# Optimization experiments

Hardware: AMD Instinct MI355X
Metric: run time of the kernel (lower is better)

The kernel has to match this reference:

```python
import jax, jax.numpy as jnp
import numpy as np

DIM = 384
HEADS = 6
NEG = -1e9  # masked-score fill; equivalent to gathering only kept K/V rows


def setup_inputs() -> dict:
    key = jax.random.key(0)
    ks = jax.random.split(key, 9)
    B, N, C = 1, 4098, DIM
    x = jax.random.normal(ks[0], (B, N, C), dtype=jnp.float32)
    pos = jax.random.normal(ks[1], (B, N + 1, C), dtype=jnp.float32)
    # float mask in [0,1); >=0.5 means 'foreground / keep as key', <0.5 pooled into back token
    mask = jax.random.uniform(ks[2], (B, 1, N - 2), dtype=jnp.float32)
    mask_block = jnp.ones((N + 1,), dtype=jnp.float32)  # positions 0, N-1, N always kept
    Wq = jax.random.normal(ks[3], (C, C), dtype=jnp.float32) * 0.02
    Wk = jax.random.normal(ks[4], (C, C), dtype=jnp.float32) * 0.02
    Wv = jax.random.normal(ks[5], (C, C), dtype=jnp.float32) * 0.02
    Wp = jax.random.normal(ks[6], (C, C), dtype=jnp.float32) * 0.02
    bp = jnp.zeros((C,), dtype=jnp.float32)
    return {"x": x, "pos": pos, "mask": mask, "mask_block": mask_block,
            "Wq": Wq, "Wk": Wk, "Wv": Wv, "Wp": Wp, "bp": bp}


def reference(x, pos, mask, mask_block, Wq, Wk, Wv, Wp, bp):
    B, N, C = x.shape
    H = HEADS
    D = C // H
    scale = D ** -0.5
    eps = 1e-10

    # back token: average of background (mask < 0.5) interior tokens
    reverse = jnp.where(mask < 0.5, 1.0, 0.0)                      # (B,1,N-2)
    pooled = jnp.einsum('bon,bnc->boc', reverse, x[:, 1:N - 1])    # (B,1,C)
    back_tokens = pooled / (reverse.sum(axis=2, keepdims=True) + eps)

    kv_x = jnp.concatenate([x, back_tokens], axis=1)               # (B,N+1,C)
    q_x = x + pos[:, :N]
    k_x = kv_x + pos

    q = (q_x @ Wq.T).reshape(B, N, H, D).transpose(0, 2, 1, 3)       # (B,H,N,D)
    k = (k_x @ Wk.T).reshape(B, N + 1, H, D).transpose(0, 2, 1, 3)   # (B,H,N+1,D)
    v = (kv_x @ Wv.T).reshape(B, N + 1, H, D).transpose(0, 2, 1, 3)  # (B,H,N+1,D)

    # key-selection mask: original gathers rows with mask_block >= 0.5;
    # masked softmax over all N+1 keys is mathematically identical.
    mb = mask_block.at[1:N - 1].set(mask[0, 0])
    keep = mb >= 0.5                                               # (N+1,)

    scores = jnp.einsum('bhqd,bhkd->bhqk', q, k) * scale
    scores = jnp.where(keep[None, None, None, :], scores, NEG)
    attn = jax.nn.softmax(scores, axis=-1)
    out = jnp.einsum('bhqk,bhkd->bhqd', attn, v)
    out = out.transpose(0, 2, 1, 3).reshape(B, N, C)
    return out @ Wp.T + bp
```

## Files before the change

kernel.cpp:

```cpp
#include <hip/hip_runtime.h>
#include <math.h>

#define N_TOK 4098
#define NK_TOK 4099
#define C_DIM 384
#define NKPAD 4160

typedef short  bh8 __attribute__((ext_vector_type(8)));
typedef float  f32x4 __attribute__((ext_vector_type(4)));
typedef unsigned short ushort;
typedef ushort u4 __attribute__((ext_vector_type(4)));
typedef ushort u8 __attribute__((ext_vector_type(8)));

static __device__ __forceinline__ ushort f2bf(float f) {
  unsigned int u = __float_as_uint(f);
  u = (u + 0x7FFF + ((u >> 16) & 1)) >> 16;
  return (ushort)u;
}
static __device__ __forceinline__ float bf2f(ushort s) {
  return __uint_as_float(((unsigned int)s) << 16);
}

typedef const __attribute__((address_space(1))) unsigned int* gas_t;
typedef __attribute__((address_space(3))) unsigned int* las_t;
static __device__ __forceinline__ void gload16(const void* g, void* l) {
  __builtin_amdgcn_global_load_lds((gas_t)g, (las_t)l, 16, 0, 0);
}

static __device__ __forceinline__ void stage_tile(const ushort* src, int rs,
                                                  ushort* lds, int t) {
#pragma unroll
  for (int it = 0; it < 2; ++it) {
    const int base = it * 256 + (t & 192);
    const int i = base + (t & 63);
    const int r = i >> 3, c8 = i & 7;
    gload16(src + r * rs + ((c8 ^ (r & 7)) << 3), lds + base * 8);
  }
}
static __device__ __forceinline__ bh8 frag(const ushort* lds, int row, int c8) {
  return *(const bh8*)&lds[(row << 6) + ((c8 ^ (row & 7)) << 3)];
}

__global__ __launch_bounds__(384) void poolkeep_kernel(
    const float* __restrict__ x, const float* __restrict__ mask,
    const float* __restrict__ mask_block, float* __restrict__ pooled,
    float* __restrict__ cnt, int* __restrict__ nk, int* __restrict__ inv) {
  const int b = blockIdx.x, t = threadIdx.x;
  if (b < 128) {
    const int r0 = b * 32;
    float acc = 0.f;
    int lc = 0;
    for (int r = r0; r < r0 + 32; ++r)
      if (mask[r] < 0.5f) { acc += x[(size_t)(r + 1) * C_DIM + t]; ++lc; }
    atomicAdd(&pooled[t], acc);
    if (t == 0) atomicAdd(cnt, (float)lc);
  } else {
    const int w = t >> 6, lane = t & 63;
    const int span = (b - 128) * 6 + w;
    if (span >= 65) return;
    const int j = span * 64 + lane;
    bool keep = false;
    if (j < NK_TOK)
      keep = (j >= 1 && j <= N_TOK - 2) ? (mask[j - 1] >= 0.5f)
                                        : (mask_block[j] >= 0.5f);
    const unsigned long long bal = __ballot(keep);
    const int pre = __popcll(bal & ((1ull << lane) - 1ull));
    const int c64 = __popcll(bal);
    int base = 0;
    if (lane == 0) base = atomicAdd(nk, c64);
    base = __shfl(base, 0);
    if (j < NK_TOK) inv[j] = keep ? (base + pre) : -1;
  }
}

__global__ __launch_bounds__(256) void prep_kernel(
    const float* __restrict__ x, const float* __restrict__ pos,
    const float* __restrict__ pooled, const float* __restrict__ cnt,
    const float* __restrict__ Wq, const float* __restrict__ Wk,
    const float* __restrict__ Wv, const float* __restrict__ Wp,
    ushort* __restrict__ Aq, ushort* __restrict__ Ak,
    ushort* __restrict__ Av, ushort* __restrict__ Wb) {
  const int b = blockIdx.x, t = threadIdx.x;
  if (b < 65) {
    const int r0 = b * 64;
#pragma unroll 4
    for (int i = 0; i < 24; ++i) {
      const int idx = i * 1024 + t * 4;
      const int row = r0 + idx / C_DIM, col = idx % C_DIM;
      if (row > NK_TOK - 1) continue;
      const float4 pv = *(const float4*)&pos[(size_t)row * C_DIM + col];
      float4 xv;
      if (row == NK_TOK - 1) {
        const float ic = 1.f / (*cnt + 1e-10f);
        xv.x = pooled[col] * ic;     xv.y = pooled[col + 1] * ic;
        xv.z = pooled[col + 2] * ic; xv.w = pooled[col + 3] * ic;
      } else {
        xv = *(const float4*)&x[(size_t)row * C_DIM + col];
      }
      if (row < N_TOK) {
        u4 q4 = {f2bf((xv.x + pv.x) * 0.125f), f2bf((xv.y + pv.y) * 0.125f),
                 f2bf((xv.z + pv.z) * 0.125f), f2bf((xv.w + pv.w) * 0.125f)};
        *(u4*)&Aq[(size_t)row * C_DIM + col] = q4;
      }
      u4 k4 = {f2bf(xv.x + pv.x), f2bf(xv.y + pv.y),
               f2bf(xv.z + pv.z), f2bf(xv.w + pv.w)};
      *(u4*)&Ak[(size_t)row * C_DIM + col] = k4;
      u4 v4 = {f2bf(xv.x), f2bf(xv.y), f2bf(xv.z), f2bf(xv.w)};
      *(u4*)&Av[(size_t)row * C_DIM + col] = v4;
    }
  } else {
    const int wi = b - 65;
    const float* src = (wi < 4) ? Wq : (wi < 8) ? Wk : (wi < 12) ? Wv : Wp;
    const int base = (wi & 3) * 36864;
#pragma unroll 4
    for (int i = 0; i < 36; ++i) {
      const int idx = base + i * 1024 + t * 4;
      const float4 v = *(const float4*)&src[idx];
      u4 o = {f2bf(v.x), f2bf(v.y), f2bf(v.z), f2bf(v.w)};
      *(u4*)&Wb[(size_t)(wi >> 2) * 147456 + idx] = o;
    }
  }
}

static __device__ __forceinline__ void gemm_core(const ushort* A, const ushort* B,
    ushort* As, ushort* Bs, int t, int w, int quad, int l15, f32x4 acc[4]) {
  stage_tile(A, C_DIM, As, t);
  stage_tile(B, C_DIM, Bs, t);
  __syncthreads();
#pragma unroll
  for (int kt = 0; kt < 6; ++kt) {
    const int cur = (kt & 1) << 12;
    if (kt < 5) {
      stage_tile(A + (kt + 1) * 64, C_DIM, As + (cur ^ 4096), t);
      stage_tile(B + (kt + 1) * 64, C_DIM, Bs + (cur ^ 4096), t);
    }
    const bh8 b0 = frag(Bs + cur, w * 16 + l15, quad);
    const bh8 b1 = frag(Bs + cur, w * 16 + l15, 4 + quad);
#pragma unroll
    for (int mb = 0; mb < 4; ++mb) {
      const bh8 a0 = frag(As + cur, mb * 16 + l15, quad);
      const bh8 a1 = frag(As + cur, mb * 16 + l15, 4 + quad);
      acc[mb] = __builtin_amdgcn_mfma_f32_16x16x32_bf16(a0, b0, acc[mb], 0, 0, 0);
      acc[mb] = __builtin_amdgcn_mfma_f32_16x16x32_bf16(a1, b1, acc[mb], 0, 0, 0);
    }
    __syncthreads();
  }
}

__global__ __launch_bounds__(256) void gemm3_kernel(
    const ushort* __restrict__ Aq, const ushort* __restrict__ Ak,
    const ushort* __restrict__ Av, const ushort* __restrict__ Wb,
    const int* __restrict__ inv, ushort* __restrict__ Qh,
    ushort* __restrict__ Kc, ushort* __restrict__ Vc) {
  __shared__ ushort As[8192], Bs[8192];
  const int t = threadIdx.x, w = t >> 6, lane = t & 63;
  const int quad = lane >> 4, l15 = lane & 15;
  const int m0 = blockIdx.x * 64;
  const int which = blockIdx.y / 6, h = blockIdx.y % 6;
  const ushort* A = (which == 0 ? Aq : which == 1 ? Ak : Av) + (size_t)m0 * C_DIM;
  const ushort* B = Wb + (size_t)which * 147456 + (size_t)h * 64 * C_DIM;
  f32x4 acc[4];
#pragma unroll
  for (int i = 0; i < 4; ++i) acc[i] = (f32x4){0.f, 0.f, 0.f, 0.f};
  gemm_core(A, B, As, Bs, t, w, quad, l15, acc);
  const int n = w * 16 + l15;
  if (which == 0) {
#pragma unroll
    for (int mb = 0; mb < 4; ++mb)
#pragma unroll
      for (int r = 0; r < 4; ++r) {
        const int m = m0 + mb * 16 + quad * 4 + r;
        if (m < N_TOK) Qh[((size_t)h * N_TOK + m) * 64 + n] = f2bf(acc[mb][r]);
      }
  } else {
    ushort* dst = (which == 1) ? Kc : Vc;
#pragma unroll
    for (int mb = 0; mb < 4; ++mb)
#pragma unroll
      for (int r = 0; r < 4; ++r) {
        const int m = m0 + mb * 16 + quad * 4 + r;
        if (m < NK_TOK) {
          const int slot = inv[m];
          if (slot >= 0) dst[((size_t)h * NKPAD + slot) * 64 + n] = f2bf(acc[mb][r]);
        }
      }
  }
}

__global__ __launch_bounds__(256) void gemm_out_kernel(
    const ushort* __restrict__ Am, const ushort* __restrict__ Wpb,
    const float* __restrict__ bp, float* __restrict__ out) {
  __shared__ ushort As[8192], Bs[8192];
  const int t = threadIdx.x, w = t >> 6, lane = t & 63;
  const int quad = lane >> 4, l15 = lane & 15;
  const int m0 = blockIdx.x * 64;
  const int h = blockIdx.y;
  f32x4 acc[4];
#pragma unroll
  for (int i = 0; i < 4; ++i) acc[i] = (f32x4){0.f, 0.f, 0.f, 0.f};
  gemm_core(Am + (size_t)m0 * C_DIM, Wpb + (size_t)h * 64 * C_DIM,
            As, Bs, t, w, quad, l15, acc);
  const int n = w * 16 + l15;
  const float bb = bp[h * 64 + n];
#pragma unroll
  for (int mb = 0; mb < 4; ++mb)
#pragma unroll
    for (int r = 0; r < 4; ++r) {
      const int m = m0 + mb * 16 + quad * 4 + r;
      if (m < N_TOK) out[(size_t)m * C_DIM + h * 64 + n] = acc[mb][r] + bb;
    }
}

__global__ __launch_bounds__(256) void vtrans_kernel(const ushort* __restrict__ Vc,
                                                     ushort* __restrict__ Vt) {
  __shared__ ushort T[64][72];
  const int c = blockIdx.x, h = blockIdx.y, t = threadIdx.x;
#pragma unroll
  for (int i = 0; i < 2; ++i) {
    const int s = t + i * 256, r = s >> 3, g = s & 7;
    *(u8*)&T[r][g * 8] =
        *(const u8*)&Vc[((size_t)h * NKPAD + c * 64 + r) * 64 + g * 8];
  }
  __syncthreads();
#pragma unroll
  for (int i = 0; i < 2; ++i) {
    const int s = t + i * 256, d = s >> 3, g = s & 7;
    u8 o;
#pragma unroll
    for (int j = 0; j < 8; ++j) o[j] = T[g * 8 + j][d];
    *(u8*)&Vt[((size_t)h * 64 + d) * NKPAD + c * 64 + g * 8] = o;
  }
}

__global__ __launch_bounds__(256) void attn_kernel(
    const ushort* __restrict__ Qh, const ushort* __restrict__ Kc,
    const ushort* __restrict__ Vt, const int* __restrict__ nkp,
    ushort* __restrict__ Opart, float* __restrict__ Lpart) {
  __shared__ ushort KsB[8192], VsB[8192];
  __shared__ ushort Ps[4][32][72];
  const int t = threadIdx.x, w = t >> 6, lane = t & 63;
  const int quad = lane >> 4, l15 = lane & 15;
  const int h = blockIdx.y, slice = blockIdx.z;
  const int q0 = blockIdx.x * 128;
  const int nk = *nkp, nchunk = (nk + 63) >> 6;

  bh8 qf[2][2];
#pragma unroll
  for (int g = 0; g < 2; ++g) {
    int qr = q0 + w * 32 + g * 16 + l15;
    if (qr > N_TOK - 1) qr = N_TOK - 1;
    const ushort* qp = Qh + ((size_t)h * N_TOK + qr) * 64 + quad * 8;
    qf[g][0] = *(const bh8*)qp;
    qf[g][1] = *(const bh8*)(qp + 32);
  }
  f32x4 oacc[2][4];
#pragma unroll
  for (int g = 0; g < 2; ++g)
#pragma unroll
    for (int i = 0; i < 4; ++i) oacc[g][i] = (f32x4){0.f, 0.f, 0.f, 0.f};
  float l_r[2] = {0.f, 0.f};

  const ushort* kb = Kc + (size_t)h * NKPAD * 64;
  const ushort* vb = Vt + (size_t)h * 64 * NKPAD;

  if (slice < nchunk) {
    stage_tile(kb + (size_t)slice * 4096, 64, KsB, t);
    stage_tile(vb + slice * 64, NKPAD, VsB, t);
  }
  __syncthreads();
  int bsel = 0;
  for (int kc = slice; kc < nchunk; kc += 3) {
    if (kc + 3 < nchunk) {
      stage_tile(kb + (size_t)(kc + 3) * 4096, 64, KsB + ((bsel ^ 1) << 12), t);
      stage_tile(vb + (kc + 3) * 64, NKPAD, VsB + ((bsel ^ 1) << 12), t);
    }
    const ushort* ks = KsB + (bsel << 12);
    const ushort* vs = VsB + (bsel << 12);
#pragma unroll
    for (int g = 0; g < 2; ++g) {
      float csum = 0.f;
#pragma unroll
      for (int f = 0; f < 4; ++f) {
        f32x4 s4 = {0.f, 0.f, 0.f, 0.f};
        const bh8 a0 = frag(ks, f * 16 + l15, quad);
        const bh8 a1 = frag(ks, f * 16 + l15, 4 + quad);
        s4 = __builtin_amdgcn_mfma_f32_16x16x32_bf16(a0, qf[g][0], s4, 0, 0, 0);
        s4 = __builtin_amdgcn_mfma_f32_16x16x32_bf16(a1, qf[g][1], s4, 0, 0, 0);
        const int keyb = kc * 64 + f * 16 + quad * 4;
        u4 pv;
#pragma unroll
        for (int r = 0; r < 4; ++r) {
          const float p = (keyb + r < nk) ? __expf(s4[r]) : 0.f;
          csum += p;
          pv[r] = f2bf(p);
        }
        *(u4*)&Ps[w][g * 16 + l15][f * 16 + quad * 4] = pv;
      }
      csum += __shfl_xor(csum, 16);
      csum += __shfl_xor(csum, 32);
      l_r[g] += csum;
    }
    bh8 pa[2][2];
#pragma unroll
    for (int g = 0; g < 2; ++g) {
      pa[g][0] = *(const bh8*)&Ps[w][g * 16 + l15][quad * 8];
      pa[g][1] = *(const bh8*)&Ps[w][g * 16 + l15][32 + quad * 8];
    }
#pragma unroll
    for (int db = 0; db < 4; ++db) {
      const bh8 b0 = frag(vs, db * 16 + l15, quad);
      const bh8 b1 = frag(vs, db * 16 + l15, 4 + quad);
#pragma unroll
      for (int g = 0; g < 2; ++g) {
        oacc[g][db] = __builtin_amdgcn_mfma_f32_16x16x32_bf16(pa[g][0], b0, oacc[g][db], 0, 0, 0);
        oacc[g][db] = __builtin_amdgcn_mfma_f32_16x16x32_bf16(pa[g][1], b1, oacc[g][db], 0, 0, 0);
      }
    }
    __syncthreads();
    bsel ^= 1;
  }
  const int sh = slice * 6 + h;
#pragma unroll
  for (int g = 0; g < 2; ++g) {
#pragma unroll
    for (int db = 0; db < 4; ++db)
#pragma unroll
      for (int r = 0; r < 4; ++r) {
        const int q = q0 + w * 32 + g * 16 + quad * 4 + r;
        if (q < N_TOK)
          Opart[((size_t)sh * NKPAD + q) * 64 + db * 16 + l15] = f2bf(oacc[g][db][r]);
      }
    if (quad == 0) {
      const int q = q0 + w * 32 + g * 16 + l15;
      if (q < N_TOK) Lpart[sh * NKPAD + q] = l_r[g];
    }
  }
}

__global__ __launch_bounds__(256) void merge_kernel(const ushort* __restrict__ Opart,
                                                    const float* __restrict__ Lpart,
                                                    ushort* __restrict__ Am) {
  const int idx = blockIdx.x * 256 + threadIdx.x;
  if (idx >= N_TOK * 48) return;
  const int q = idx / 48, c = (idx % 48) * 8;
  const int h = c >> 6, d = c & 63;
  float l = 0.f;
#pragma unroll
  for (int s = 0; s < 3; ++s) l += Lpart[(s * 6 + h) * NKPAD + q];
  const float inv = 1.f / l;
  float o[8] = {0.f, 0.f, 0.f, 0.f, 0.f, 0.f, 0.f, 0.f};
#pragma unroll
  for (int s = 0; s < 3; ++s) {
    const u8 v = *(const u8*)&Opart[((size_t)(s * 6 + h) * NKPAD + q) * 64 + d];
#pragma unroll
    for (int j = 0; j < 8; ++j) o[j] += bf2f(v[j]);
  }
  u8 r;
#pragma unroll
  for (int j = 0; j < 8; ++j) r[j] = f2bf(o[j] * inv);
  *(u8*)&Am[(size_t)q * C_DIM + c] = r;
}

extern "C" void kernel_launch(void* const* d_in, const int* in_sizes, int n_in,
                              void* d_out, int out_size, void* d_ws, size_t ws_size,
                              hipStream_t stream) {
  const float* x          = (const float*)d_in[0];
  const float* pos        = (const float*)d_in[1];
  const float* mask       = (const float*)d_in[2];
  const float* mask_block = (const float*)d_in[3];
  const float* Wq         = (const float*)d_in[4];
  const float* Wk         = (const float*)d_in[5];
  const float* Wv         = (const float*)d_in[6];
  const float* Wp         = (const float*)d_in[7];
  const float* bp         = (const float*)d_in[8];
  float* out = (float*)d_out;
  char* wsb = (char*)d_ws;

  float*  pooled = (float*)wsb;
  float*  cnt    = (float*)(wsb + 1536);
  int*    nk     = (int*)(wsb + 1540);
  int*    inv    = (int*)(wsb + 2048);
  ushort* Aq     = (ushort*)(wsb + 20480);
  ushort* Ak     = (ushort*)(wsb + 3215360);
  ushort* Av     = (ushort*)(wsb + 6410240);
  ushort* Wb     = (ushort*)(wsb + 9605120);
  ushort* Qh     = (ushort*)(wsb + 10784768);
  ushort* Kc     = (ushort*)(wsb + 13932032);
  ushort* Vc     = (ushort*)(wsb + 17126912);
  ushort* Vt     = (ushort*)(wsb + 20321792);
  float*  Lp     = (float*)(wsb + 23516672);
  ushort* Am     = (ushort*)(wsb + 23816192);
  ushort* Op     = Aq;

  hipMemsetAsync(d_ws, 0, 2048, stream);
  poolkeep_kernel<<<dim3(139), dim3(384), 0, stream>>>(x, mask, mask_block,
                                                       pooled, cnt, nk, inv);
  prep_kernel<<<dim3(81), dim3(256), 0, stream>>>(x, pos, pooled, cnt,
                                                  Wq, Wk, Wv, Wp, Aq, Ak, Av, Wb);
  gemm3_kernel<<<dim3(65, 18), 256, 0, stream>>>(Aq, Ak, Av, Wb, inv, Qh, Kc, Vc);
  vtrans_kernel<<<dim3(65, 6), 256, 0, stream>>>(Vc, Vt);
  attn_kernel<<<dim3(33, 6, 3), 256, 0, stream>>>(Qh, Kc, Vt, nk, Op, Lp);
  merge_kernel<<<dim3(769), 256, 0, stream>>>(Op, Lp, Am);
  gemm_out_kernel<<<dim3(65, 6), 256, 0, stream>>>(Am, Wb + 3 * 147456, bp, out);
}
```

Before: 166.2 us.

## Cut kernel launches: fuse V transpose, merge into attention, drop memset and atomics

Removes the memset, the V-transpose kernel and the merge kernel. gemm3 now writes V directly in transposed layout, and the last attention slice block for each (q-tile, head) does the 3-way partial merge, chosen through an atomic counter with threadfences. Pooling now writes per-block partials that prep reduces. The keep-index scan moves into prep as a block-level prefix sum, and prep uses more, smaller blocks. This saves launch overhead and intermediate round trips, at the cost of strided scattered stores for Vt and a serial pooled reduction in one prep block, which the other 255 row blocks do not wait on (block 256 alone handles the back-token row).

```diff
diff --git a/kernel.cpp b/kernel.cpp
--- a/kernel.cpp
+++ b/kernel.cpp
@@ -41,62 +41,57 @@
   return *(const bh8*)&lds[(row << 6) + ((c8 ^ (row & 7)) << 3)];
 }
 
-__global__ __launch_bounds__(384) void poolkeep_kernel(
+__global__ __launch_bounds__(384) void pool_kernel(
     const float* __restrict__ x, const float* __restrict__ mask,
-    const float* __restrict__ mask_block, float* __restrict__ pooled,
-    float* __restrict__ cnt, int* __restrict__ nk, int* __restrict__ inv) {
+    float* __restrict__ pooled_part, float* __restrict__ cnt_part,
+    int* __restrict__ done) {
   const int b = blockIdx.x, t = threadIdx.x;
-  if (b < 128) {
-    const int r0 = b * 32;
-    float acc = 0.f;
-    int lc = 0;
-    for (int r = r0; r < r0 + 32; ++r)
-      if (mask[r] < 0.5f) { acc += x[(size_t)(r + 1) * C_DIM + t]; ++lc; }
-    atomicAdd(&pooled[t], acc);
-    if (t == 0) atomicAdd(cnt, (float)lc);
-  } else {
-    const int w = t >> 6, lane = t & 63;
-    const int span = (b - 128) * 6 + w;
-    if (span >= 65) return;
-    const int j = span * 64 + lane;
-    bool keep = false;
-    if (j < NK_TOK)
-      keep = (j >= 1 && j <= N_TOK - 2) ? (mask[j - 1] >= 0.5f)
-                                        : (mask_block[j] >= 0.5f);
-    const unsigned long long bal = __ballot(keep);
-    const int pre = __popcll(bal & ((1ull << lane) - 1ull));
-    const int c64 = __popcll(bal);
-    int base = 0;
-    if (lane == 0) base = atomicAdd(nk, c64);
-    base = __shfl(base, 0);
-    if (j < NK_TOK) inv[j] = keep ? (base + pre) : -1;
-  }
+  if (b == 128) { if (t < 198) done[t] = 0; return; }
+  const int r0 = b * 32;
+  float acc = 0.f;
+  int lc = 0;
+  for (int r = r0; r < r0 + 32; ++r)
+    if (mask[r] < 0.5f) { acc += x[(size_t)(r + 1) * C_DIM + t]; ++lc; }
+  pooled_part[b * C_DIM + t] = acc;
+  if (t == 0) cnt_part[b] = (float)lc;
 }
 
 __global__ __launch_bounds__(256) void prep_kernel(
     const float* __restrict__ x, const float* __restrict__ pos,
-    const float* __restrict__ pooled, const float* __restrict__ cnt,
+    const float* __restrict__ pooled_part, const float* __restrict__ cnt_part,
     const float* __restrict__ Wq, const float* __restrict__ Wk,
     const float* __restrict__ Wv, const float* __restrict__ Wp,
-    ushort* __restrict__ Aq, ushort* __restrict__ Ak,
-    ushort* __restrict__ Av, ushort* __restrict__ Wb) {
+    const float* __restrict__ mask, const float* __restrict__ mask_block,
+    ushort* __restrict__ Aq, ushort* __restrict__ Ak, ushort* __restrict__ Av,
+    ushort* __restrict__ Wb, int* __restrict__ nk, int* __restrict__ inv) {
   const int b = blockIdx.x, t = threadIdx.x;
-  if (b < 65) {
-    const int r0 = b * 64;
-#pragma unroll 4
-    for (int i = 0; i < 24; ++i) {
+  if (b < 260) {
+    __shared__ float sback[C_DIM];
+    if (b == 256) {
+      float cs = 0.f;
+      for (int i = (t & 63); i < 128; i += 64) cs += cnt_part[i];
+#pragma unroll
+      for (int d = 1; d < 64; d <<= 1) cs += __shfl_xor(cs, d);
+      const float ic = 1.f / (cs + 1e-10f);
+      for (int c = t; c < C_DIM; c += 256) {
+        float s = 0.f;
+        for (int p = 0; p < 128; ++p) s += pooled_part[p * C_DIM + c];
+        sback[c] = s * ic;
+      }
+      __syncthreads();
+    }
+    const int r0 = b * 16;
+#pragma unroll
+    for (int i = 0; i < 6; ++i) {
       const int idx = i * 1024 + t * 4;
       const int row = r0 + idx / C_DIM, col = idx % C_DIM;
-      if (row > NK_TOK - 1) continue;
+      if (row >= NK_TOK) continue;
       const float4 pv = *(const float4*)&pos[(size_t)row * C_DIM + col];
       float4 xv;
-      if (row == NK_TOK - 1) {
-        const float ic = 1.f / (*cnt + 1e-10f);
-        xv.x = pooled[col] * ic;     xv.y = pooled[col + 1] * ic;
-        xv.z = pooled[col + 2] * ic; xv.w = pooled[col + 3] * ic;
-      } else {
+      if (row == NK_TOK - 1)
+        xv = make_float4(sback[col], sback[col + 1], sback[col + 2], sback[col + 3]);
+      else
         xv = *(const float4*)&x[(size_t)row * C_DIM + col];
-      }
       if (row < N_TOK) {
         u4 q4 = {f2bf((xv.x + pv.x) * 0.125f), f2bf((xv.y + pv.y) * 0.125f),
                  f2bf((xv.z + pv.z) * 0.125f), f2bf((xv.w + pv.w) * 0.125f)};
@@ -108,16 +103,46 @@
       u4 v4 = {f2bf(xv.x), f2bf(xv.y), f2bf(xv.z), f2bf(xv.w)};
       *(u4*)&Av[(size_t)row * C_DIM + col] = v4;
     }
+  } else if (b < 292) {
+    const int wi = b - 260;
+    const float* src = (wi < 8) ? Wq : (wi < 16) ? Wk : (wi < 24) ? Wv : Wp;
+    const int base = (wi >> 3) * 147456 + (wi & 7) * 18432;
+#pragma unroll 2
+    for (int i = 0; i < 18; ++i) {
+      const int g = base + i * 1024 + t * 4;
+      const float4 v = *(const float4*)&src[g - (wi >> 3) * 147456 + 0];
+      u4 o = {f2bf(v.x), f2bf(v.y), f2bf(v.z), f2bf(v.w)};
+      *(u4*)&Wb[g] = o;
+    }
   } else {
-    const int wi = b - 65;
-    const float* src = (wi < 4) ? Wq : (wi < 8) ? Wk : (wi < 12) ? Wv : Wp;
-    const int base = (wi & 3) * 36864;
-#pragma unroll 4
-    for (int i = 0; i < 36; ++i) {
-      const int idx = base + i * 1024 + t * 4;
-      const float4 v = *(const float4*)&src[idx];
-      u4 o = {f2bf(v.x), f2bf(v.y), f2bf(v.z), f2bf(v.w)};
-      *(u4*)&Wb[(size_t)(wi >> 2) * 147456 + idx] = o;
+    __shared__ int scnt[256];
+    const int j0 = t * 17;
+    unsigned int bits = 0;
+    int c = 0;
+#pragma unroll 1
+    for (int u = 0; u < 17; ++u) {
+      const int j = j0 + u;
+      bool keep = false;
+      if (j < NK_TOK)
+        keep = (j >= 1 && j <= N_TOK - 2) ? (mask[j - 1] >= 0.5f)
+                                          : (mask_block[j] >= 0.5f);
+      if (keep) { bits |= 1u << u; ++c; }
+    }
+    scnt[t] = c;
+    __syncthreads();
+    for (int d = 1; d < 256; d <<= 1) {
+      const int v = scnt[t];
+      const int add = (t >= d) ? scnt[t - d] : 0;
+      __syncthreads();
+      scnt[t] = v + add;
+      __syncthreads();
+    }
+    int base = scnt[t] - c;
+    if (t == 255) *nk = scnt[255];
+#pragma unroll 1
+    for (int u = 0; u < 17; ++u) {
+      const int j = j0 + u;
+      if (j < NK_TOK) inv[j] = ((bits >> u) & 1) ? base++ : -1;
     }
   }
 }
@@ -151,7 +176,7 @@
     const ushort* __restrict__ Aq, const ushort* __restrict__ Ak,
     const ushort* __restrict__ Av, const ushort* __restrict__ Wb,
     const int* __restrict__ inv, ushort* __restrict__ Qh,
-    ushort* __restrict__ Kc, ushort* __restrict__ Vc) {
+    ushort* __restrict__ Kc, ushort* __restrict__ Vt) {
   __shared__ ushort As[8192], Bs[8192];
   const int t = threadIdx.x, w = t >> 6, lane = t & 63;
   const int quad = lane >> 4, l15 = lane & 15;
@@ -172,8 +197,7 @@
         const int m = m0 + mb * 16 + quad * 4 + r;
         if (m < N_TOK) Qh[((size_t)h * N_TOK + m) * 64 + n] = f2bf(acc[mb][r]);
       }
-  } else {
-    ushort* dst = (which == 1) ? Kc : Vc;
+  } else if (which == 1) {
 #pragma unroll
     for (int mb = 0; mb < 4; ++mb)
 #pragma unroll
@@ -181,7 +205,18 @@
         const int m = m0 + mb * 16 + quad * 4 + r;
         if (m < NK_TOK) {
           const int slot = inv[m];
-          if (slot >= 0) dst[((size_t)h * NKPAD + slot) * 64 + n] = f2bf(acc[mb][r]);
+          if (slot >= 0) Kc[((size_t)h * NKPAD + slot) * 64 + n] = f2bf(acc[mb][r]);
+        }
+      }
+  } else {
+#pragma unroll
+    for (int mb = 0; mb < 4; ++mb)
+#pragma unroll
+      for (int r = 0; r < 4; ++r) {
+        const int m = m0 + mb * 16 + quad * 4 + r;
+        if (m < NK_TOK) {
+          const int slot = inv[m];
+          if (slot >= 0) Vt[((size_t)h * 64 + n) * NKPAD + slot] = f2bf(acc[mb][r]);
         }
       }
   }
@@ -211,33 +246,14 @@
     }
 }
 
-__global__ __launch_bounds__(256) void vtrans_kernel(const ushort* __restrict__ Vc,
-                                                     ushort* __restrict__ Vt) {
-  __shared__ ushort T[64][72];
-  const int c = blockIdx.x, h = blockIdx.y, t = threadIdx.x;
-#pragma unroll
-  for (int i = 0; i < 2; ++i) {
-    const int s = t + i * 256, r = s >> 3, g = s & 7;
-    *(u8*)&T[r][g * 8] =
-        *(const u8*)&Vc[((size_t)h * NKPAD + c * 64 + r) * 64 + g * 8];
-  }
-  __syncthreads();
-#pragma unroll
-  for (int i = 0; i < 2; ++i) {
-    const int s = t + i * 256, d = s >> 3, g = s & 7;
-    u8 o;
-#pragma unroll
-    for (int j = 0; j < 8; ++j) o[j] = T[g * 8 + j][d];
-    *(u8*)&Vt[((size_t)h * 64 + d) * NKPAD + c * 64 + g * 8] = o;
-  }
-}
-
 __global__ __launch_bounds__(256) void attn_kernel(
     const ushort* __restrict__ Qh, const ushort* __restrict__ Kc,
     const ushort* __restrict__ Vt, const int* __restrict__ nkp,
-    ushort* __restrict__ Opart, float* __restrict__ Lpart) {
+    ushort* __restrict__ Opart, float* __restrict__ Lpart,
+    int* __restrict__ done, ushort* __restrict__ Am) {
   __shared__ ushort KsB[8192], VsB[8192];
   __shared__ ushort Ps[4][32][72];
+  __shared__ int sdone;
   const int t = threadIdx.x, w = t >> 6, lane = t & 63;
   const int quad = lane >> 4, l15 = lane & 15;
   const int h = blockIdx.y, slice = blockIdx.z;
@@ -335,30 +351,33 @@
       if (q < N_TOK) Lpart[sh * NKPAD + q] = l_r[g];
     }
   }
-}
-
-__global__ __launch_bounds__(256) void merge_kernel(const ushort* __restrict__ Opart,
-                                                    const float* __restrict__ Lpart,
-                                                    ushort* __restrict__ Am) {
-  const int idx = blockIdx.x * 256 + threadIdx.x;
-  if (idx >= N_TOK * 48) return;
-  const int q = idx / 48, c = (idx % 48) * 8;
-  const int h = c >> 6, d = c & 63;
-  float l = 0.f;
-#pragma unroll
-  for (int s = 0; s < 3; ++s) l += Lpart[(s * 6 + h) * NKPAD + q];
-  const float inv = 1.f / l;
-  float o[8] = {0.f, 0.f, 0.f, 0.f, 0.f, 0.f, 0.f, 0.f};
-#pragma unroll
-  for (int s = 0; s < 3; ++s) {
-    const u8 v = *(const u8*)&Opart[((size_t)(s * 6 + h) * NKPAD + q) * 64 + d];
-#pragma unroll
-    for (int j = 0; j < 8; ++j) o[j] += bf2f(v[j]);
-  }
-  u8 r;
-#pragma unroll
-  for (int j = 0; j < 8; ++j) r[j] = f2bf(o[j] * inv);
-  *(u8*)&Am[(size_t)q * C_DIM + c] = r;
+
+  __threadfence();
+  if (t == 0) sdone = atomicAdd(&done[blockIdx.x * 6 + h], 1);
+  __syncthreads();
+  if (sdone != 2) return;
+  __threadfence();
+#pragma unroll
+  for (int i = 0; i < 4; ++i) {
+    const int q = q0 + i * 32 + (t >> 3);
+    if (q >= N_TOK) continue;
+    const int d = (t & 7) * 8;
+    float l = 0.f;
+#pragma unroll
+    for (int s = 0; s < 3; ++s) l += Lpart[(s * 6 + h) * NKPAD + q];
+    const float invl = 1.f / l;
+    float o[8] = {0.f, 0.f, 0.f, 0.f, 0.f, 0.f, 0.f, 0.f};
+#pragma unroll
+    for (int s = 0; s < 3; ++s) {
+      const u8 v = *(const u8*)&Opart[((size_t)(s * 6 + h) * NKPAD + q) * 64 + d];
+#pragma unroll
+      for (int j = 0; j < 8; ++j) o[j] += bf2f(v[j]);
+    }
+    u8 rr;
+#pragma unroll
+    for (int j = 0; j < 8; ++j) rr[j] = f2bf(o[j] * invl);
+    *(u8*)&Am[(size_t)q * C_DIM + h * 64 + d] = rr;
+  }
 }
 
 extern "C" void kernel_launch(void* const* d_in, const int* in_sizes, int n_in,
@@ -376,30 +395,28 @@
   float* out = (float*)d_out;
   char* wsb = (char*)d_ws;
 
-  float*  pooled = (float*)wsb;
-  float*  cnt    = (float*)(wsb + 1536);
-  int*    nk     = (int*)(wsb + 1540);
-  int*    inv    = (int*)(wsb + 2048);
-  ushort* Aq     = (ushort*)(wsb + 20480);
-  ushort* Ak     = (ushort*)(wsb + 3215360);
-  ushort* Av     = (ushort*)(wsb + 6410240);
-  ushort* Wb     = (ushort*)(wsb + 9605120);
-  ushort* Qh     = (ushort*)(wsb + 10784768);
-  ushort* Kc     = (ushort*)(wsb + 13932032);
-  ushort* Vc     = (ushort*)(wsb + 17126912);
-  ushort* Vt     = (ushort*)(wsb + 20321792);
-  float*  Lp     = (float*)(wsb + 23516672);
-  ushort* Am     = (ushort*)(wsb + 23816192);
-  ushort* Op     = Aq;
-
-  hipMemsetAsync(d_ws, 0, 2048, stream);
-  poolkeep_kernel<<<dim3(139), dim3(384), 0, stream>>>(x, mask, mask_block,
-                                                       pooled, cnt, nk, inv);
-  prep_kernel<<<dim3(81), dim3(256), 0, stream>>>(x, pos, pooled, cnt,
-                                                  Wq, Wk, Wv, Wp, Aq, Ak, Av, Wb);
-  gemm3_kernel<<<dim3(65, 18), 256, 0, stream>>>(Aq, Ak, Av, Wb, inv, Qh, Kc, Vc);
-  vtrans_kernel<<<dim3(65, 6), 256, 0, stream>>>(Vc, Vt);
-  attn_kernel<<<dim3(33, 6, 3), 256, 0, stream>>>(Qh, Kc, Vt, nk, Op, Lp);
-  merge_kernel<<<dim3(769), 256, 0, stream>>>(Op, Lp, Am);
+  float*  pooled_part = (float*)wsb;
+  float*  cnt_part    = (float*)(wsb + 196608);
+  int*    nk          = (int*)(wsb + 197120);
+  int*    done        = (int*)(wsb + 197632);
+  int*    inv         = (int*)(wsb + 198656);
+  ushort* Aq          = (ushort*)(wsb + 215296);
+  ushort* Ak          = (ushort*)(wsb + 3410176);
+  ushort* Av          = (ushort*)(wsb + 6605056);
+  ushort* Wb          = (ushort*)(wsb + 9799936);
+  ushort* Qh          = (ushort*)(wsb + 10979584);
+  ushort* Kc          = (ushort*)(wsb + 14126848);
+  ushort* Vt          = (ushort*)(wsb + 17321728);
+  float*  Lp          = (float*)(wsb + 20516608);
+  ushort* Am          = (ushort*)(wsb + 20816128);
+  ushort* Op          = Aq;
+
+  pool_kernel<<<dim3(129), dim3(384), 0, stream>>>(x, mask, pooled_part,
+                                                   cnt_part, done);
+  prep_kernel<<<dim3(293), dim3(256), 0, stream>>>(x, pos, pooled_part, cnt_part,
+                                                   Wq, Wk, Wv, Wp, mask, mask_block,
+                                                   Aq, Ak, Av, Wb, nk, inv);
+  gemm3_kernel<<<dim3(65, 18), 256, 0, stream>>>(Aq, Ak, Av, Wb, inv, Qh, Kc, Vt);
+  attn_kernel<<<dim3(33, 6, 3), 256, 0, stream>>>(Qh, Kc, Vt, nk, Op, Lp, done, Am);
   gemm_out_kernel<<<dim3(65, 6), 256, 0, stream>>>(Am, Wb + 3 * 147456, bp, out);
 }
```

Result: slower. 252.2 us (+51.8%).
